# Kernel tuning notes

Hardware: AMD Instinct MI355X
Metric: run time of the kernel (lower is better)

The kernel has to match this reference:

```python
import jax, jax.numpy as jnp
import numpy as np

B, P, CD, RD, H, NR, OD, T = 1024, 22, 256, 64, 512, 12, 2, 100
IN = OD + 2 + CD + RD  # 324: [pos(2), ball(2), context(256), role_embed(64)]


def setup_inputs() -> dict:
    key = jax.random.key(0)
    ks = jax.random.split(key, 20)
    def n(k, shape, s=1.0):
        return jax.random.normal(k, shape, dtype=jnp.float32) * s
    sH = 1.0 / np.sqrt(H)
    sI = 1.0 / np.sqrt(IN)
    return {
        "context": n(ks[0], (B, P, CD)),
        "initial_position": n(ks[1], (B, P, OD)),
        "ball_landing": n(ks[2], (B, 2)),
        "roles": jax.random.randint(ks[3], (B, P), 0, NR, dtype=jnp.int32),
        "max_steps": T,
        "role_table": n(ks[4], (NR, RD), 0.02),
        # LSTM layer 0 (input_dim=IN)
        "W_ih0": n(ks[5], (4 * H, IN), sI),
        "W_hh0": n(ks[6], (4 * H, H), sH),
        "b0": n(ks[7], (4 * H,), sH),  # b_ih + b_hh fused
        # LSTM layer 1 (input_dim=H)
        "W_ih1": n(ks[8], (4 * H, H), sH),
        "W_hh1": n(ks[9], (4 * H, H), sH),
        "b1": n(ks[10], (4 * H,), sH),
        # output MLP: H -> H//2 -> OD
        "W_fc1": n(ks[11], (H // 2, H), sH),
        "b_fc1": n(ks[12], (H // 2,), sH),
        "W_fc2": n(ks[13], (OD, H // 2), 1.0 / np.sqrt(H // 2)),
        "b_fc2": n(ks[14], (OD,), 0.02),
        # initial_pos_encoder: Linear(OD, H)
        "W_init": n(ks[15], (H, OD), 1.0 / np.sqrt(OD)),
        "b_init": n(ks[16], (H,), 0.02),
    }


def _lstm_cell(x, h, c, W_ih, W_hh, b):
    # PyTorch gate order: i, f, g, o
    gates = x @ W_ih.T + h @ W_hh.T + b  # [N, 4H]
    i, f, g, o = jnp.split(gates, 4, axis=-1)
    c_new = jax.nn.sigmoid(f) * c + jax.nn.sigmoid(i) * jnp.tanh(g)
    h_new = jax.nn.sigmoid(o) * jnp.tanh(c_new)
    return h_new, c_new


def reference(context, initial_position, ball_landing, roles, max_steps,
              role_table, W_ih0, W_hh0, b0, W_ih1, W_hh1, b1,
              W_fc1, b_fc1, W_fc2, b_fc2, W_init, b_init):
    batch, num_players, context_dim = context.shape
    N = batch * num_players
    out_dim = initial_position.shape[-1]

    ctx_flat = context.reshape(N, context_dim)
    role_flat = role_table[roles].reshape(N, -1)
    ball_flat = jnp.broadcast_to(ball_landing[:, None, :], (batch, num_players, 2)).reshape(N, 2)
    static = jnp.concatenate([ball_flat, ctx_flat, role_flat], axis=1)  # [N, IN-2]

    pos0 = initial_position.reshape(N, out_dim)
    h0 = pos0 @ W_init.T + b_init  # initial_pos_encoder into layer-0 hidden
    c0 = jnp.zeros_like(h0)
    h1 = jnp.zeros_like(h0)
    c1 = jnp.zeros_like(h0)

    def step(carry, _):
        pos, h0, c0, h1, c1 = carry
        x = jnp.concatenate([pos, static], axis=1)  # [N, IN]
        h0, c0 = _lstm_cell(x, h0, c0, W_ih0, W_hh0, b0)
        h1, c1 = _lstm_cell(h0, h1, c1, W_ih1, W_hh1, b1)
        # output MLP (dropout inactive in eval)
        nxt = jax.nn.relu(h1 @ W_fc1.T + b_fc1) @ W_fc2.T + b_fc2  # [N, OD]
        return (nxt, h0, c0, h1, c1), nxt

    _, preds = jax.lax.scan(step, (pos0, h0, c0, h1, c1), None, length=max_steps)
    # preds: [T, N, OD] -> [batch, num_players, T, OD]
    preds = preds.transpose(1, 0, 2).reshape(batch, num_players, max_steps, out_dim)
    return preds
```

## Files before the change

kernel.cpp:

```cpp
#include <hip/hip_runtime.h>
#include <cstdint>


#define DEVI __device__ __forceinline__

typedef __bf16 bf16x8 __attribute__((ext_vector_type(8)));
typedef float  f32x4  __attribute__((ext_vector_type(4)));
typedef float  f32x2  __attribute__((ext_vector_type(2)));
typedef unsigned short u16x4 __attribute__((ext_vector_type(4)));

static constexpr int NROWS = 22528;
static constexpr int T_STEPS = 100;
static constexpr int NBM = 176;

DEVI unsigned short f2bf(float f) {
  unsigned u = __float_as_uint(f);
  u = u + 0x7FFFu + ((u >> 16) & 1u);
  return (unsigned short)(u >> 16);
}
DEVI float bf2f(unsigned short h) { return __uint_as_float(((unsigned)h) << 16); }

DEVI float fast_sigmoid(float x) {
  float e = __builtin_amdgcn_exp2f(-1.442695041f * x);
  return __builtin_amdgcn_rcpf(1.0f + e);
}
DEVI float fast_tanh(float x) {
  float e = __builtin_amdgcn_exp2f(2.885390082f * x);
  return 1.0f - 2.0f * __builtin_amdgcn_rcpf(e + 1.0f);
}

DEVI void async_copy16(const void* g, void* l) {
  __builtin_amdgcn_global_load_lds(
      (const __attribute__((address_space(1))) void*)g,
      (__attribute__((address_space(3))) void*)l, 16, 0, 0);
}

template <int KITERS, int KSWITCH>
DEVI void gemm_core(const unsigned short* __restrict__ A1, int lda1,
                    const unsigned short* __restrict__ A2, int lda2,
                    const unsigned short* __restrict__ B1, int ldb1,
                    const unsigned short* __restrict__ B2, int ldb2,
                    unsigned short* lds, f32x4 acc[4][4], int tid) {
  const int lane = tid & 63, wid = tid >> 6;
  const int wm = wid & 1, wn = wid >> 1;
  const int c16 = lane & 15, q = lane >> 4;
#pragma unroll
  for (int i = 0; i < 4; ++i)
#pragma unroll
    for (int j = 0; j < 4; ++j) acc[i][j] = f32x4{0.f, 0.f, 0.f, 0.f};
#pragma unroll
  for (int kt = 0; kt < KITERS; ++kt) {
    const bool sec = (kt >= KSWITCH);
    const unsigned short* Ab = sec ? A2 : A1;
    const unsigned short* Bb = sec ? B2 : B1;
    const int lda = sec ? lda2 : lda1;
    const int ldb = sec ? ldb2 : ldb1;
    const int kk = (sec ? (kt - KSWITCH) : kt) * 64;
    __syncthreads();
#pragma unroll
    for (int rd = 0; rd < 4; ++rd) {
      int p = rd * 256 + tid;
      int row = p >> 3, u = p & 7, ch = u ^ (row & 7);
      async_copy16(Ab + row * lda + kk + ch * 8, lds + p * 8);
      async_copy16(Bb + row * ldb + kk + ch * 8, lds + 8192 + p * 8);
    }
    __syncthreads();
#pragma unroll
    for (int s = 0; s < 2; ++s) {
      bf16x8 a[4], b[4];
#pragma unroll
      for (int mf = 0; mf < 4; ++mf) {
        int row = wm * 64 + mf * 16 + c16;
        int slot = row * 8 + ((s * 4 + q) ^ (row & 7));
        a[mf] = *(const bf16x8*)(lds + slot * 8);
      }
#pragma unroll
      for (int nf = 0; nf < 4; ++nf) {
        int row = wn * 64 + nf * 16 + c16;
        int slot = row * 8 + ((s * 4 + q) ^ (row & 7));
        b[nf] = *(const bf16x8*)(lds + 8192 + slot * 8);
      }
#pragma unroll
      for (int mf = 0; mf < 4; ++mf)
#pragma unroll
        for (int nf = 0; nf < 4; ++nf)
          acc[mf][nf] = __builtin_amdgcn_mfma_f32_16x16x32_bf16(a[mf], b[nf], acc[mf][nf], 0, 0, 0);
    }
  }
}

DEVI int orig_row(int j) {
  int tile = j >> 7, rem = j & 127;
  int half = rem >> 6, g = (rem >> 4) & 3, cc = rem & 15;
  return g * 512 + (tile * 32 + half * 16 + cc);
}

__global__ void k_prep_w(const float* __restrict__ Whh0, const float* __restrict__ Wih1,
                         const float* __restrict__ Whh1, const float* __restrict__ Wih0,
                         const float* __restrict__ Wfc1, const float* __restrict__ b0,
                         const float* __restrict__ b1,
                         unsigned short* __restrict__ W0p, unsigned short* __restrict__ Wc1p,
                         unsigned short* __restrict__ Wsp, unsigned short* __restrict__ Wfc1b,
                         float* __restrict__ Wposx, float* __restrict__ Wposy,
                         float* __restrict__ b0p4, float* __restrict__ b1p4) {
  int j = blockIdx.x;
  int k = threadIdx.x;
  int o = orig_row(j);
  W0p[j * 512 + k]         = f2bf(Whh0[o * 512 + k]);
  Wc1p[j * 1024 + k]       = f2bf(Wih1[o * 512 + k]);
  Wc1p[j * 1024 + 512 + k] = f2bf(Whh1[o * 512 + k]);
  if (k < 384) Wsp[j * 384 + k] = (k < 322) ? f2bf(Wih0[o * 324 + 2 + k]) : (unsigned short)0;
  if (k == 0) {
    int g = (j >> 4) & 3;
    int cg = (j >> 7) * 32 + ((j >> 6) & 1) * 16 + (j & 15);
    Wposx[cg * 4 + g] = Wih0[o * 324 + 0];
    Wposy[cg * 4 + g] = Wih0[o * 324 + 1];
    b0p4[cg * 4 + g] = b0[o];
    b1p4[cg * 4 + g] = b1[o];
  }
  if (j < 256) Wfc1b[j * 512 + k] = f2bf(Wfc1[j * 512 + k]);
}

__global__ void k_init_xs(const float* __restrict__ ball, const float* __restrict__ ctx,
                          const int* __restrict__ roles, const float* __restrict__ role_table,
                          unsigned short* __restrict__ Xs) {
  int n = blockIdx.x, col = threadIdx.x;
  int b = n / 22;
  float v;
  if (col < 2)        v = ball[b * 2 + col];
  else if (col < 258) v = ctx[(size_t)n * 256 + col - 2];
  else if (col < 322) v = role_table[roles[n] * 64 + col - 258];
  else                v = 0.f;
  Xs[(size_t)n * 384 + col] = f2bf(v);
}

__global__ void k_init_state(const float* __restrict__ pos0, const float* __restrict__ Winit,
                             const float* __restrict__ binit, unsigned short* __restrict__ Hcat,
                             float* __restrict__ c0, float* __restrict__ c1,
                             float* __restrict__ posb) {
  int idx = blockIdx.x * 256 + threadIdx.x;
  if (idx >= NROWS * 512) return;
  int n = idx >> 9, c = idx & 511;
  float px = pos0[n * 2 + 0], py = pos0[n * 2 + 1];
  float h0 = binit[c] + Winit[c * 2 + 0] * px + Winit[c * 2 + 1] * py;
  Hcat[(size_t)n * 1024 + c] = f2bf(h0);
  Hcat[(size_t)n * 1024 + 512 + c] = 0;
  c0[idx] = 0.f;
  c1[idx] = 0.f;
  if (c < 2) posb[n * 2 + c] = pos0[n * 2 + c];
}

__global__ __launch_bounds__(256) void k_static(const unsigned short* __restrict__ Xs,
                                                const unsigned short* __restrict__ Wsp,
                                                const float* __restrict__ b0p4,
                                                unsigned short* __restrict__ SP2) {
  __shared__ __align__(16) unsigned short lds[16384];
  int tid = threadIdx.x, bn = blockIdx.x, bm = blockIdx.y;
  f32x4 acc[4][4];
  const unsigned short* Ab = Xs + (size_t)bm * 128 * 384;
  const unsigned short* Bb = Wsp + (size_t)bn * 128 * 384;
  gemm_core<6, 6>(Ab, 384, Ab, 384, Bb, 384, Bb, 384, lds, acc, tid);
  int lane = tid & 63, wid = tid >> 6, wm = wid & 1, wn = wid >> 1;
  int c16 = lane & 15, q = lane >> 4;
  int cg = bn * 32 + wn * 16 + c16;
  f32x4 bb = *(const f32x4*)&b0p4[cg * 4];
#pragma unroll
  for (int mf = 0; mf < 4; ++mf) {
    int row0 = bm * 128 + wm * 64 + mf * 16 + q * 4;
#pragma unroll
    for (int r = 0; r < 4; ++r) {
      u16x4 v;
      v.x = f2bf(acc[mf][0][r] + bb.x);
      v.y = f2bf(acc[mf][1][r] + bb.y);
      v.z = f2bf(acc[mf][2][r] + bb.z);
      v.w = f2bf(acc[mf][3][r] + bb.w);
      ((u16x4*)SP2)[(size_t)(row0 + r) * 512 + cg] = v;
    }
  }
}


struct GemmSrc {
  const unsigned short *A1, *A2, *B1, *B2;
  int ldA1, ldA2, ldB1, ldB2;
};

template <int KT, int KSW>
DEVI void stage_q(const GemmSrc& g, int t, int s, int isB, unsigned short* dst, int tid) {
  int tt = (t >= KT) ? (t - 2) : t;
  const bool sec = (tt >= KSW);
  const unsigned short* base;
  int ld;
  if (isB) { base = sec ? g.B2 : g.B1; ld = sec ? g.ldB2 : g.ldB1; }
  else     { base = sec ? g.A2 : g.A1; ld = sec ? g.ldA2 : g.ldA1; }
  base += (sec ? (tt - KSW) : tt) * 64 + s * 32;
#pragma unroll
  for (int rd = 0; rd < 2; ++rd) {
    int p = rd * 512 + tid;
    int row = p >> 2, u = p & 3, ch = u ^ ((row >> 1) & 3);
    async_copy16(base + row * ld + ch * 8, dst + p * 8);
  }
}

#define GBAR   asm volatile("s_barrier" ::: "memory")
#define VMCNT4 asm volatile("s_waitcnt vmcnt(4)" ::: "memory")

template <int KT, int KSW>
DEVI void gemm8(const GemmSrc& g, unsigned short* lds, f32x4 acc[8][4], int tid) {
  const int lane = tid & 63, wid = tid >> 6;
  const int wm = wid >> 2, wn = wid & 3;
  const int c16 = lane & 15, q = lane >> 4;
#pragma unroll
  for (int i = 0; i < 8; ++i)
#pragma unroll
    for (int j = 0; j < 4; ++j) acc[i][j] = f32x4{0.f, 0.f, 0.f, 0.f};
  unsigned short* A00 = lds;
  unsigned short* A01 = lds + 8192;
  unsigned short* B00 = lds + 16384;
  unsigned short* B01 = lds + 24576;
  unsigned short* A10 = lds + 32768;
  unsigned short* A11 = lds + 40960;
  unsigned short* B10 = lds + 49152;
  unsigned short* B11 = lds + 57344;
  const int rowA0 = wm * 128 + c16;
  const int rowB0 = wn * 64 + c16;
  stage_q<KT, KSW>(g, 0, 0, 0, A00, tid);
  stage_q<KT, KSW>(g, 0, 0, 1, B00, tid);
  stage_q<KT, KSW>(g, 0, 1, 0, A01, tid);
  stage_q<KT, KSW>(g, 0, 1, 1, B01, tid);
  stage_q<KT, KSW>(g, 1, 0, 0, A10, tid);
  stage_q<KT, KSW>(g, 1, 0, 1, B10, tid);
  VMCNT4;
  GBAR;
  bf16x8 a[4], b[4];

#define LOADA(BASE, MG)                                                        \
  _Pragma("unroll")                                                            \
  for (int f = 0; f < 4; ++f) {                                                \
    int row = rowA0 + ((MG) * 4 + f) * 16;                                     \
    a[f] = *(const bf16x8*)((BASE) + (row * 4 + (q ^ ((row >> 1) & 3))) * 8);  \
  }
#define LOADB(BASE)                                                            \
  _Pragma("unroll")                                                            \
  for (int f = 0; f < 4; ++f) {                                                \
    int row = rowB0 + f * 16;                                                  \
    b[f] = *(const bf16x8*)((BASE) + (row * 4 + (q ^ ((row >> 1) & 3))) * 8);  \
  }
#define MFG(MG)                                                                \
  __builtin_amdgcn_s_setprio(1);                                               \
  _Pragma("unroll")                                                            \
  for (int f = 0; f < 4; ++f)                                                  \
    _Pragma("unroll")                                                          \
    for (int nf = 0; nf < 4; ++nf)                                             \
      acc[(MG) * 4 + f][nf] = __builtin_amdgcn_mfma_f32_16x16x32_bf16(         \
          a[f], b[nf], acc[(MG) * 4 + f][nf], 0, 0, 0);                        \
  __builtin_amdgcn_s_setprio(0);                                               \
  __builtin_amdgcn_sched_barrier(0);

#pragma unroll 1
  for (int it = 0; it < KT / 2; ++it) {
    const int t0 = 2 * it;
    LOADA(A00, 0); LOADB(B00);
    stage_q<KT, KSW>(g, t0 + 1, 1, 0, A11, tid);
    GBAR; MFG(0); GBAR;
    LOADA(A00, 1);
    stage_q<KT, KSW>(g, t0 + 1, 1, 1, B11, tid);
    GBAR; MFG(1); GBAR;
    LOADA(A01, 0); LOADB(B01);
    stage_q<KT, KSW>(g, t0 + 2, 0, 0, A00, tid);
    GBAR; MFG(0); GBAR;
    LOADA(A01, 1);
    stage_q<KT, KSW>(g, t0 + 2, 0, 1, B00, tid);
    GBAR; MFG(1); VMCNT4; GBAR;
    LOADA(A10, 0); LOADB(B10);
    stage_q<KT, KSW>(g, t0 + 2, 1, 0, A01, tid);
    GBAR; MFG(0); GBAR;
    LOADA(A10, 1);
    stage_q<KT, KSW>(g, t0 + 2, 1, 1, B01, tid);
    GBAR; MFG(1); GBAR;
    LOADA(A11, 0); LOADB(B11);
    stage_q<KT, KSW>(g, t0 + 3, 0, 0, A10, tid);
    GBAR; MFG(0); GBAR;
    LOADA(A11, 1);
    stage_q<KT, KSW>(g, t0 + 3, 0, 1, B10, tid);
    GBAR; MFG(1); VMCNT4; GBAR;
  }
  asm volatile("s_waitcnt vmcnt(0)" ::: "memory");
#undef LOADA
#undef LOADB
#undef MFG
}

DEVI void swz704(int l, int& bn, int& bm) {
  int xcd = l & 7, ii = l >> 3;
  bn = ii & 7;
  bm = (ii >> 3) * 8 + xcd;
}

template <bool USE_SP>
__global__ __launch_bounds__(512, 2) void k_s1_8(const unsigned short* __restrict__ cur,
                                                 const unsigned short* __restrict__ Xs,
                                                 const unsigned short* __restrict__ W0p,
                                                 const unsigned short* __restrict__ Wsp,
                                                 const unsigned short* __restrict__ SP2,
                                                 const float* __restrict__ b0p4,
                                                 const float* __restrict__ Wposx,
                                                 const float* __restrict__ Wposy,
                                                 const float* __restrict__ posb,
                                                 float* __restrict__ c0,
                                                 unsigned short* __restrict__ nxt) {
  __shared__ __align__(16) unsigned short lds[65536];
  const int tid = threadIdx.x;
  int bn, bm;
  swz704(blockIdx.x, bn, bm);
  f32x4 acc[8][4];
  GemmSrc g;
  g.A1 = cur + (size_t)bm * 256 * 1024; g.ldA1 = 1024;
  g.B1 = W0p + (size_t)bn * 256 * 512;  g.ldB1 = 512;
  if constexpr (USE_SP) {
    g.A2 = g.A1; g.ldA2 = 1024; g.B2 = g.B1; g.ldB2 = 512;
    gemm8<8, 8>(g, lds, acc, tid);
  } else {
    g.A2 = Xs + (size_t)bm * 256 * 384;  g.ldA2 = 384;
    g.B2 = Wsp + (size_t)bn * 256 * 384; g.ldB2 = 384;
    gemm8<14, 8>(g, lds, acc, tid);
  }
  const int lane = tid & 63, wid = tid >> 6;
  const int wm = wid >> 2, wn = wid & 3;
  const int c16 = lane & 15, q = lane >> 4;
  const int cg = bn * 64 + (wn >> 1) * 32 + (wn & 1) * 16 + c16;
  f32x4 wpx = *(const f32x4*)&Wposx[cg * 4];
  f32x4 wpy = *(const f32x4*)&Wposy[cg * 4];
  f32x4 sb = f32x4{0.f, 0.f, 0.f, 0.f};
  if constexpr (!USE_SP) sb = *(const f32x4*)&b0p4[cg * 4];
#pragma unroll
  for (int mf = 0; mf < 8; ++mf) {
    int row0 = bm * 256 + wm * 128 + mf * 16 + q * 4;
    f32x4 cold = *(const f32x4*)&c0[(size_t)cg * NROWS + row0];
    f32x4 cnew;
#pragma unroll
    for (int r = 0; r < 4; ++r) {
      size_t row = row0 + r;
      f32x2 pv = *(const f32x2*)&posb[row * 2];
      float s0 = sb.x, s1 = sb.y, s2 = sb.z, s3 = sb.w;
      if constexpr (USE_SP) {
        u16x4 sp = ((const u16x4*)SP2)[row * 512 + cg];
        s0 = bf2f(sp.x); s1 = bf2f(sp.y); s2 = bf2f(sp.z); s3 = bf2f(sp.w);
      }
      float gi = acc[mf][0][r] + s0 + pv.x * wpx.x + pv.y * wpy.x;
      float gf = acc[mf][1][r] + s1 + pv.x * wpx.y + pv.y * wpy.y;
      float gg = acc[mf][2][r] + s2 + pv.x * wpx.z + pv.y * wpy.z;
      float go = acc[mf][3][r] + s3 + pv.x * wpx.w + pv.y * wpy.w;
      float cn = fast_sigmoid(gf) * cold[r] + fast_sigmoid(gi) * fast_tanh(gg);
      cnew[r] = cn;
      nxt[row * 1024 + cg] = f2bf(fast_sigmoid(go) * fast_tanh(cn));
    }
    *(f32x4*)&c0[(size_t)cg * NROWS + row0] = cnew;
  }
}

__global__ __launch_bounds__(512, 2) void k_s2_8(const unsigned short* __restrict__ nxt_in,
                                                 const unsigned short* __restrict__ cur,
                                                 const unsigned short* __restrict__ Wc1p,
                                                 const float* __restrict__ b1p4,
                                                 float* __restrict__ c1,
                                                 unsigned short* __restrict__ nxt_out) {
  __shared__ __align__(16) unsigned short lds[65536];
  const int tid = threadIdx.x;
  int bn, bm;
  swz704(blockIdx.x, bn, bm);
  f32x4 acc[8][4];
  GemmSrc g;
  g.A1 = nxt_in + (size_t)bm * 256 * 1024;      g.ldA1 = 1024;
  g.A2 = cur + (size_t)bm * 256 * 1024 + 512;   g.ldA2 = 1024;
  g.B1 = Wc1p + (size_t)bn * 256 * 1024;        g.ldB1 = 1024;
  g.B2 = g.B1 + 512;                            g.ldB2 = 1024;
  gemm8<16, 8>(g, lds, acc, tid);
  const int lane = tid & 63, wid = tid >> 6;
  const int wm = wid >> 2, wn = wid & 3;
  const int c16 = lane & 15, q = lane >> 4;
  const int cg = bn * 64 + (wn >> 1) * 32 + (wn & 1) * 16 + c16;
  f32x4 bv = *(const f32x4*)&b1p4[cg * 4];
#pragma unroll
  for (int mf = 0; mf < 8; ++mf) {
    int row0 = bm * 256 + wm * 128 + mf * 16 + q * 4;
    f32x4 cold = *(const f32x4*)&c1[(size_t)cg * NROWS + row0];
    f32x4 cnew;
#pragma unroll
    for (int r = 0; r < 4; ++r) {
      size_t row = row0 + r;
      float gi = acc[mf][0][r] + bv.x;
      float gf = acc[mf][1][r] + bv.y;
      float gg = acc[mf][2][r] + bv.z;
      float go = acc[mf][3][r] + bv.w;
      float cn = fast_sigmoid(gf) * cold[r] + fast_sigmoid(gi) * fast_tanh(gg);
      cnew[r] = cn;
      nxt_out[row * 1024 + 512 + cg] = f2bf(fast_sigmoid(go) * fast_tanh(cn));
    }
    *(f32x4*)&c1[(size_t)cg * NROWS + row0] = cnew;
  }
}

__global__ __launch_bounds__(256) void k_s3(const unsigned short* __restrict__ H,
                                            const unsigned short* __restrict__ Wfc1b,
                                            const float* __restrict__ bfc1,
                                            const float* __restrict__ Wfc2,
                                            const float* __restrict__ bfc2,
                                            float* __restrict__ out, float* __restrict__ posb,
                                            int t) {
  __shared__ __align__(16) unsigned short ldsA[32 * 64];
  __shared__ __align__(16) unsigned short ldsB[256 * 64];
  __shared__ float wfc2s[512];
  __shared__ float red[32 * 8];
  int tid = threadIdx.x;
  int l = blockIdx.x, xcd = l & 7, i = l >> 3;
  int b32 = 4 * (xcd + 8 * (i >> 2)) + (i & 3);
  wfc2s[tid] = Wfc2[tid];
  wfc2s[tid + 256] = Wfc2[tid + 256];
  int lane = tid & 63, wid = tid >> 6;
  int c16 = lane & 15, q = lane >> 4;
  f32x4 acc[2][4];
#pragma unroll
  for (int ii = 0; ii < 2; ++ii)
#pragma unroll
    for (int jj = 0; jj < 4; ++jj) acc[ii][jj] = f32x4{0.f, 0.f, 0.f, 0.f};
  const unsigned short* Ab = H + (size_t)b32 * 32 * 1024 + 512;
#pragma unroll
  for (int kt = 0; kt < 8; ++kt) {
    int k0 = kt * 64;
    __syncthreads();
    {
      int p = tid;
      int row = p >> 3, u = p & 7, ch = u ^ (row & 7);
      async_copy16(Ab + row * 1024 + k0 + ch * 8, ldsA + p * 8);
    }
#pragma unroll
    for (int rd = 0; rd < 8; ++rd) {
      int p = rd * 256 + tid;
      int row = p >> 3, u = p & 7, ch = u ^ (row & 7);
      async_copy16(Wfc1b + row * 512 + k0 + ch * 8, ldsB + p * 8);
    }
    __syncthreads();
#pragma unroll
    for (int s = 0; s < 2; ++s) {
      bf16x8 a[2], b[4];
#pragma unroll
      for (int mf = 0; mf < 2; ++mf) {
        int row = mf * 16 + c16;
        int slot = row * 8 + ((s * 4 + q) ^ (row & 7));
        a[mf] = *(const bf16x8*)(ldsA + slot * 8);
      }
#pragma unroll
      for (int nf = 0; nf < 4; ++nf) {
        int row = wid * 64 + nf * 16 + c16;
        int slot = row * 8 + ((s * 4 + q) ^ (row & 7));
        b[nf] = *(const bf16x8*)(ldsB + slot * 8);
      }
#pragma unroll
      for (int mf = 0; mf < 2; ++mf)
#pragma unroll
        for (int nf = 0; nf < 4; ++nf)
          acc[mf][nf] = __builtin_amdgcn_mfma_f32_16x16x32_bf16(a[mf], b[nf], acc[mf][nf], 0, 0, 0);
    }
  }
  float part[2][2][4];
#pragma unroll
  for (int d = 0; d < 2; ++d)
#pragma unroll
    for (int mf = 0; mf < 2; ++mf)
#pragma unroll
      for (int r = 0; r < 4; ++r) part[d][mf][r] = 0.f;
#pragma unroll
  for (int nf = 0; nf < 4; ++nf) {
    int col = wid * 64 + nf * 16 + c16;
    float w0 = wfc2s[col], w1 = wfc2s[256 + col], bv = bfc1[col];
#pragma unroll
    for (int mf = 0; mf < 2; ++mf)
#pragma unroll
      for (int r = 0; r < 4; ++r) {
        float v = acc[mf][nf][r] + bv;
        v = v > 0.f ? v : 0.f;
        part[0][mf][r] += v * w0;
        part[1][mf][r] += v * w1;
      }
  }
#pragma unroll
  for (int st = 1; st < 16; st <<= 1)
#pragma unroll
    for (int d = 0; d < 2; ++d)
#pragma unroll
      for (int mf = 0; mf < 2; ++mf)
#pragma unroll
        for (int r = 0; r < 4; ++r)
          part[d][mf][r] += __shfl_xor(part[d][mf][r], st, 64);
  if (c16 == 0) {
#pragma unroll
    for (int mf = 0; mf < 2; ++mf)
#pragma unroll
      for (int r = 0; r < 4; ++r) {
        int rl = mf * 16 + q * 4 + r;
        red[rl * 8 + wid * 2 + 0] = part[0][mf][r];
        red[rl * 8 + wid * 2 + 1] = part[1][mf][r];
      }
  }
  __syncthreads();
  if (tid < 64) {
    int rl = tid >> 1, d = tid & 1;
    float s = red[rl * 8 + d] + red[rl * 8 + 2 + d] + red[rl * 8 + 4 + d]
            + red[rl * 8 + 6 + d] + bfc2[d];
    int rg = b32 * 32 + rl;
    out[((size_t)rg * T_STEPS + t) * 2 + d] = s;
    posb[rg * 2 + d] = s;
  }
}

extern "C" void kernel_launch(void* const* d_in, const int* in_sizes, int n_in,
                              void* d_out, int out_size, void* d_ws, size_t ws_size,
                              hipStream_t stream) {
  (void)in_sizes; (void)n_in; (void)out_size;
  const float* ctx   = (const float*)d_in[0];
  const float* pos0  = (const float*)d_in[1];
  const float* ball  = (const float*)d_in[2];
  const int*   roles = (const int*)d_in[3];
  const float* role_table = (const float*)d_in[5];
  const float* Wih0 = (const float*)d_in[6];
  const float* Whh0 = (const float*)d_in[7];
  const float* b0   = (const float*)d_in[8];
  const float* Wih1 = (const float*)d_in[9];
  const float* Whh1 = (const float*)d_in[10];
  const float* b1   = (const float*)d_in[11];
  const float* Wfc1 = (const float*)d_in[12];
  const float* bfc1 = (const float*)d_in[13];
  const float* Wfc2 = (const float*)d_in[14];
  const float* bfc2 = (const float*)d_in[15];
  const float* Winit = (const float*)d_in[16];
  const float* binit = (const float*)d_in[17];
  float* out = (float*)d_out;

  char* w = (char*)d_ws;
  size_t used = 0;
  auto alloc = [&](size_t bytes) {
    char* p = w + used;
    used += (bytes + 255) & ~(size_t)255;
    return p;
  };
  unsigned short* W0p   = (unsigned short*)alloc((size_t)2048 * 512 * 2);
  unsigned short* Wc1p  = (unsigned short*)alloc((size_t)2048 * 1024 * 2);
  unsigned short* Wfc1b = (unsigned short*)alloc((size_t)256 * 512 * 2);
  float* Wposx = (float*)alloc(2048 * 4);
  float* Wposy = (float*)alloc(2048 * 4);
  float* b0p4  = (float*)alloc(2048 * 4);
  float* b1p4  = (float*)alloc(2048 * 4);
  float* posb  = (float*)alloc((size_t)NROWS * 2 * 4);
  unsigned short* Hc0 = (unsigned short*)alloc((size_t)NROWS * 1024 * 2);
  float* c0   = (float*)alloc((size_t)NROWS * 512 * 4);
  float* c1   = (float*)alloc((size_t)NROWS * 512 * 4);
  unsigned short* Hc1 = (unsigned short*)alloc((size_t)NROWS * 1024 * 2);

  const size_t SP_BYTES = (size_t)NROWS * 2048 * 2;
  const bool use_sp = (ws_size >= used + SP_BYTES + (1u << 20));

  unsigned short *Xs, *Wsp, *SP2;
  if (use_sp) {
    SP2 = (unsigned short*)alloc(SP_BYTES);
    Xs  = Hc1;
    Wsp = Hc1 + (size_t)NROWS * 384;
  } else {
    SP2 = Hc1;
    Xs  = (unsigned short*)alloc((size_t)NROWS * 384 * 2);
    Wsp = (unsigned short*)alloc((size_t)2048 * 384 * 2);
  }

  k_prep_w<<<2048, 512, 0, stream>>>(Whh0, Wih1, Whh1, Wih0, Wfc1, b0, b1,
                                     W0p, Wc1p, Wsp, Wfc1b, Wposx, Wposy, b0p4, b1p4);
  k_init_xs<<<NROWS, 384, 0, stream>>>(ball, ctx, roles, role_table, Xs);
  k_init_state<<<(NROWS * 512 + 255) / 256, 256, 0, stream>>>(pos0, Winit, binit, Hc0, c0, c1, posb);

  if (use_sp) {
    dim3 gs(16, NBM);
    k_static<<<gs, 256, 0, stream>>>(Xs, Wsp, b0p4, SP2);
  }

  for (int t = 0; t < T_STEPS; ++t) {
    unsigned short* cur = (t & 1) ? Hc1 : Hc0;
    unsigned short* nxt = (t & 1) ? Hc0 : Hc1;
    if (use_sp)
      k_s1_8<true><<<704, 512, 0, stream>>>(cur, Xs, W0p, Wsp, SP2, b0p4,
                                            Wposx, Wposy, posb, c0, nxt);
    else
      k_s1_8<false><<<704, 512, 0, stream>>>(cur, Xs, W0p, Wsp, SP2, b0p4,
                                             Wposx, Wposy, posb, c0, nxt);
    k_s2_8<<<704, 512, 0, stream>>>(nxt, cur, Wc1p, b1p4, c1, nxt);
    k_s3<<<704, 256, 0, stream>>>(nxt, Wfc1b, bfc1, Wfc2, bfc2, out, posb, t);
  }
}
```

Measured before the change: 21.78 ms.

## Prefetch epilogue cell state and SP tiles into LDS during final GEMM iteration

Peels the last K-iteration of the pipelined GEMM. Its now-free stage slots issue async copies of the epilogue operands (the c0/c1 cell-state tile, or the precomputed SP2 static-gate tile) into swizzled LDS. The epilogue then reads these from LDS instead of issuing scattered global loads after the GEMM, so their latency overlaps the last MFMAs. It adds swizzle indexing complexity, a trailing __syncthreads, and a partial fallback to global loads for SP rows that did not fit in LDS.

```diff
diff --git a/kernel.cpp b/kernel.cpp
--- a/kernel.cpp
+++ b/kernel.cpp
@@ -202,11 +202,27 @@
   }
 }
 
+template <int CH0, int W0, int SH, int SH_X>
+DEVI void stage_epi(const char* base, size_t str, unsigned short* lds, int tid) {
+  constexpr int MSK = (1 << SH) - 1;
+  constexpr int MSK_X = (1 << (10 - SH_X < 5 ? 5 : 5)) - 1;
+  (void)MSK_X;
+#pragma unroll
+  for (int rd = 0; rd < 2; ++rd) {
+    int p = rd * 512 + tid;
+    int pos = CH0 + p;
+    int c = pos ^ ((pos >> SH_X) & ((1 << SH_X) - 1) & 31);
+    const char* src = base + (size_t)(c >> SH) * str + (size_t)(c & MSK) * 16;
+    async_copy16(src, lds + W0 + p * 8);
+  }
+}
+
 #define GBAR   asm volatile("s_barrier" ::: "memory")
 #define VMCNT4 asm volatile("s_waitcnt vmcnt(4)" ::: "memory")
 
-template <int KT, int KSW>
-DEVI void gemm8(const GemmSrc& g, unsigned short* lds, f32x4 acc[8][4], int tid) {
+template <int KT, int KSW, int NEPI, int ESH, int ESHX>
+DEVI void gemm8(const GemmSrc& g, const char* eb, size_t estr,
+                unsigned short* lds, f32x4 acc[8][4], int tid) {
   const int lane = tid & 63, wid = tid >> 6;
   const int wm = wid >> 2, wn = wid & 3;
   const int c16 = lane & 15, q = lane >> 4;
@@ -258,7 +274,7 @@
   __builtin_amdgcn_sched_barrier(0);
 
 #pragma unroll 1
-  for (int it = 0; it < KT / 2; ++it) {
+  for (int it = 0; it < KT / 2 - 1; ++it) {
     const int t0 = 2 * it;
     LOADA(A00, 0); LOADB(B00);
     stage_q<KT, KSW>(g, t0 + 1, 1, 0, A11, tid);
@@ -285,7 +301,41 @@
     stage_q<KT, KSW>(g, t0 + 3, 0, 1, B10, tid);
     GBAR; MFG(1); VMCNT4; GBAR;
   }
+  {
+    const int t0 = KT - 2;
+    LOADA(A00, 0); LOADB(B00);
+    stage_q<KT, KSW>(g, t0 + 1, 1, 0, A11, tid);
+    GBAR; MFG(0); GBAR;
+    LOADA(A00, 1);
+    stage_q<KT, KSW>(g, t0 + 1, 1, 1, B11, tid);
+    GBAR; MFG(1); GBAR;
+    LOADA(A01, 0); LOADB(B01);
+    if constexpr (NEPI > 0) stage_epi<0, 0, ESH, ESHX>(eb, estr, lds, tid);
+    else stage_q<KT, KSW>(g, t0 + 2, 0, 0, A00, tid);
+    GBAR; MFG(0); GBAR;
+    LOADA(A01, 1);
+    if constexpr (NEPI > 1) stage_epi<2048, 16384, ESH, ESHX>(eb, estr, lds, tid);
+    else stage_q<KT, KSW>(g, t0 + 2, 0, 1, B00, tid);
+    GBAR; MFG(1); VMCNT4; GBAR;
+    LOADA(A10, 0); LOADB(B10);
+    if constexpr (NEPI > 2) stage_epi<1024, 8192, ESH, ESHX>(eb, estr, lds, tid);
+    else stage_q<KT, KSW>(g, t0 + 2, 1, 0, A01, tid);
+    GBAR; MFG(0); GBAR;
+    LOADA(A10, 1);
+    if constexpr (NEPI > 3) stage_epi<3072, 24576, ESH, ESHX>(eb, estr, lds, tid);
+    else stage_q<KT, KSW>(g, t0 + 2, 1, 1, B01, tid);
+    GBAR; MFG(1); GBAR;
+    LOADA(A11, 0); LOADB(B11);
+    if constexpr (NEPI > 4) stage_epi<4096, 32768, ESH, ESHX>(eb, estr, lds, tid);
+    else stage_q<KT, KSW>(g, t0 + 3, 0, 0, A10, tid);
+    GBAR; MFG(0); GBAR;
+    LOADA(A11, 1);
+    if constexpr (NEPI > 5) stage_epi<5120, 49152, ESH, ESHX>(eb, estr, lds, tid);
+    else stage_q<KT, KSW>(g, t0 + 3, 0, 1, B10, tid);
+    GBAR; MFG(1); VMCNT4; GBAR;
+  }
   asm volatile("s_waitcnt vmcnt(0)" ::: "memory");
+  __syncthreads();
 #undef LOADA
 #undef LOADB
 #undef MFG
@@ -296,6 +346,8 @@
   bn = ii & 7;
   bm = (ii >> 3) * 8 + xcd;
 }
+
+DEVI int epi_word(int j) { return (j < 5) ? (j << 13) : 49152; }
 
 template <bool USE_SP>
 __global__ __launch_bounds__(512, 2) void k_s1_8(const unsigned short* __restrict__ cur,
@@ -319,16 +371,19 @@
   g.B1 = W0p + (size_t)bn * 256 * 512;  g.ldB1 = 512;
   if constexpr (USE_SP) {
     g.A2 = g.A1; g.ldA2 = 1024; g.B2 = g.B1; g.ldB2 = 512;
-    gemm8<8, 8>(g, lds, acc, tid);
+    const char* eb = (const char*)SP2 + ((size_t)(bm * 256) * 512 + (size_t)bn * 64) * 8;
+    gemm8<8, 8, 6, 5, 5>(g, eb, 4096, lds, acc, tid);
   } else {
     g.A2 = Xs + (size_t)bm * 256 * 384;  g.ldA2 = 384;
     g.B2 = Wsp + (size_t)bn * 256 * 384; g.ldB2 = 384;
-    gemm8<14, 8>(g, lds, acc, tid);
+    const char* eb = (const char*)c0 + ((size_t)bn * 64 * NROWS + (size_t)bm * 256) * 4;
+    gemm8<14, 8, 4, 6, 6>(g, eb, (size_t)NROWS * 4, lds, acc, tid);
   }
   const int lane = tid & 63, wid = tid >> 6;
   const int wm = wid >> 2, wn = wid & 3;
   const int c16 = lane & 15, q = lane >> 4;
-  const int cg = bn * 64 + (wn >> 1) * 32 + (wn & 1) * 16 + c16;
+  const int cgl = (wn >> 1) * 32 + (wn & 1) * 16 + c16;
+  const int cg = bn * 64 + cgl;
   f32x4 wpx = *(const f32x4*)&Wposx[cg * 4];
   f32x4 wpy = *(const f32x4*)&Wposy[cg * 4];
   f32x4 sb = f32x4{0.f, 0.f, 0.f, 0.f};
@@ -336,7 +391,14 @@
 #pragma unroll
   for (int mf = 0; mf < 8; ++mf) {
     int row0 = bm * 256 + wm * 128 + mf * 16 + q * 4;
-    f32x4 cold = *(const f32x4*)&c0[(size_t)cg * NROWS + row0];
+    f32x4 cold;
+    if constexpr (USE_SP) {
+      cold = *(const f32x4*)&c0[(size_t)cg * NROWS + row0];
+    } else {
+      int cc = cgl * 64 + wm * 32 + mf * 4 + q;
+      int pos = cc ^ ((cc >> 6) & 63 & 31);
+      cold = *(const f32x4*)(lds + epi_word(pos >> 10) + (pos & 1023) * 8);
+    }
     f32x4 cnew;
 #pragma unroll
     for (int r = 0; r < 4; ++r) {
@@ -344,7 +406,15 @@
       f32x2 pv = *(const f32x2*)&posb[row * 2];
       float s0 = sb.x, s1 = sb.y, s2 = sb.z, s3 = sb.w;
       if constexpr (USE_SP) {
-        u16x4 sp = ((const u16x4*)SP2)[row * 512 + cg];
+        u16x4 sp;
+        if (!(wm == 1 && mf >= 4)) {
+          int lrow = wm * 128 + mf * 16 + q * 4 + r;
+          int cc = lrow * 32 + (cgl >> 1);
+          int pos = cc ^ ((cc >> 5) & 31);
+          sp = *(const u16x4*)(lds + epi_word(pos >> 10) + (pos & 1023) * 8 + ((cgl & 1) << 2));
+        } else {
+          sp = ((const u16x4*)SP2)[row * 512 + cg];
+        }
         s0 = bf2f(sp.x); s1 = bf2f(sp.y); s2 = bf2f(sp.z); s3 = bf2f(sp.w);
       }
       float gi = acc[mf][0][r] + s0 + pv.x * wpx.x + pv.y * wpy.x;
@@ -375,16 +445,20 @@
   g.A2 = cur + (size_t)bm * 256 * 1024 + 512;   g.ldA2 = 1024;
   g.B1 = Wc1p + (size_t)bn * 256 * 1024;        g.ldB1 = 1024;
   g.B2 = g.B1 + 512;                            g.ldB2 = 1024;
-  gemm8<16, 8>(g, lds, acc, tid);
+  const char* eb = (const char*)c1 + ((size_t)bn * 64 * NROWS + (size_t)bm * 256) * 4;
+  gemm8<16, 8, 4, 6, 6>(g, eb, (size_t)NROWS * 4, lds, acc, tid);
   const int lane = tid & 63, wid = tid >> 6;
   const int wm = wid >> 2, wn = wid & 3;
   const int c16 = lane & 15, q = lane >> 4;
-  const int cg = bn * 64 + (wn >> 1) * 32 + (wn & 1) * 16 + c16;
+  const int cgl = (wn >> 1) * 32 + (wn & 1) * 16 + c16;
+  const int cg = bn * 64 + cgl;
   f32x4 bv = *(const f32x4*)&b1p4[cg * 4];
 #pragma unroll
   for (int mf = 0; mf < 8; ++mf) {
     int row0 = bm * 256 + wm * 128 + mf * 16 + q * 4;
-    f32x4 cold = *(const f32x4*)&c1[(size_t)cg * NROWS + row0];
+    int cc = cgl * 64 + wm * 32 + mf * 4 + q;
+    int pos = cc ^ ((cc >> 6) & 63 & 31);
+    f32x4 cold = *(const f32x4*)(lds + epi_word(pos >> 10) + (pos & 1023) * 8);
     f32x4 cnew;
 #pragma unroll
     for (int r = 0; r < 4; ++r) {
```

Measured after the change: 21.87 ms. No clear change (+0.4%).

## Fuse per-step LSTM kernels into one persistent cooperative kernel with grid syncs

Applied to the files above, without the earlier changes.

Replaces the 300 per-timestep kernel launches (layer-0 cell, layer-1 cell, output MLP) with a single cooperative kernel of 256 blocks. It loops over all timesteps and separates the stages with grid-wide syncs and thread fences. Stage bodies become noinline device functions, and blocks stride over the 704 GEMM tiles and 352 MLP tile pairs. This removes launch gaps, but runs one 512-thread block per CU instead of up to two, adds grid-barrier cost, and may hurt register allocation through the noinline calls. It falls back to the old launch loop if the cooperative launch fails.

```diff
diff --git a/kernel.cpp b/kernel.cpp
--- a/kernel.cpp
+++ b/kernel.cpp
@@ -1,5 +1,8 @@
 #include <hip/hip_runtime.h>
+#include <hip/hip_cooperative_groups.h>
 #include <cstdint>
+
+namespace cg = cooperative_groups;
 
 
 #define DEVI __device__ __forceinline__
@@ -178,7 +181,6 @@
     }
   }
 }
-
 
 struct GemmSrc {
   const unsigned short *A1, *A2, *B1, *B2;
@@ -298,21 +300,14 @@
 }
 
 template <bool USE_SP>
-__global__ __launch_bounds__(512, 2) void k_s1_8(const unsigned short* __restrict__ cur,
-                                                 const unsigned short* __restrict__ Xs,
-                                                 const unsigned short* __restrict__ W0p,
-                                                 const unsigned short* __restrict__ Wsp,
-                                                 const unsigned short* __restrict__ SP2,
-                                                 const float* __restrict__ b0p4,
-                                                 const float* __restrict__ Wposx,
-                                                 const float* __restrict__ Wposy,
-                                                 const float* __restrict__ posb,
-                                                 float* __restrict__ c0,
-                                                 unsigned short* __restrict__ nxt) {
-  __shared__ __align__(16) unsigned short lds[65536];
-  const int tid = threadIdx.x;
+__device__ __attribute__((noinline)) void s1_tile(
+    int l, const unsigned short* cur, const unsigned short* Xs,
+    const unsigned short* W0p, const unsigned short* Wsp,
+    const unsigned short* SP2, const float* b0p4,
+    const float* Wposx, const float* Wposy, const float* posb,
+    float* c0, unsigned short* nxt, unsigned short* lds, int tid) {
   int bn, bm;
-  swz704(blockIdx.x, bn, bm);
+  swz704(l, bn, bm);
   f32x4 acc[8][4];
   GemmSrc g;
   g.A1 = cur + (size_t)bm * 256 * 1024; g.ldA1 = 1024;
@@ -359,16 +354,12 @@
   }
 }
 
-__global__ __launch_bounds__(512, 2) void k_s2_8(const unsigned short* __restrict__ nxt_in,
-                                                 const unsigned short* __restrict__ cur,
-                                                 const unsigned short* __restrict__ Wc1p,
-                                                 const float* __restrict__ b1p4,
-                                                 float* __restrict__ c1,
-                                                 unsigned short* __restrict__ nxt_out) {
-  __shared__ __align__(16) unsigned short lds[65536];
-  const int tid = threadIdx.x;
+__device__ __attribute__((noinline)) void s2_tile(
+    int l, const unsigned short* nxt_in, const unsigned short* cur,
+    const unsigned short* Wc1p, const float* b1p4, float* c1,
+    unsigned short* nxt_out, unsigned short* lds, int tid) {
   int bn, bm;
-  swz704(blockIdx.x, bn, bm);
+  swz704(l, bn, bm);
   f32x4 acc[8][4];
   GemmSrc g;
   g.A1 = nxt_in + (size_t)bm * 256 * 1024;      g.ldA1 = 1024;
@@ -401,23 +392,17 @@
   }
 }
 
-__global__ __launch_bounds__(256) void k_s3(const unsigned short* __restrict__ H,
-                                            const unsigned short* __restrict__ Wfc1b,
-                                            const float* __restrict__ bfc1,
-                                            const float* __restrict__ Wfc2,
-                                            const float* __restrict__ bfc2,
-                                            float* __restrict__ out, float* __restrict__ posb,
-                                            int t) {
-  __shared__ __align__(16) unsigned short ldsA[32 * 64];
-  __shared__ __align__(16) unsigned short ldsB[256 * 64];
-  __shared__ float wfc2s[512];
-  __shared__ float red[32 * 8];
-  int tid = threadIdx.x;
-  int l = blockIdx.x, xcd = l & 7, i = l >> 3;
-  int b32 = 4 * (xcd + 8 * (i >> 2)) + (i & 3);
-  wfc2s[tid] = Wfc2[tid];
-  wfc2s[tid + 256] = Wfc2[tid + 256];
-  int lane = tid & 63, wid = tid >> 6;
+__device__ __attribute__((noinline)) void s3_tile(
+    int b32, const unsigned short* H, const unsigned short* Wfc1b,
+    const float* bfc1, const float* Wfc2, const float* bfc2,
+    float* out, float* posb, int t, unsigned short* ldsI, int t256) {
+  unsigned short* ldsA = ldsI;
+  unsigned short* ldsB = ldsI + 2048;
+  float* wfc2s = (float*)(ldsI + 2048 + 16384);
+  float* red   = wfc2s + 512;
+  wfc2s[t256] = Wfc2[t256];
+  wfc2s[t256 + 256] = Wfc2[t256 + 256];
+  int lane = t256 & 63, wid = t256 >> 6;
   int c16 = lane & 15, q = lane >> 4;
   f32x4 acc[2][4];
 #pragma unroll
@@ -430,13 +415,13 @@
     int k0 = kt * 64;
     __syncthreads();
     {
-      int p = tid;
+      int p = t256;
       int row = p >> 3, u = p & 7, ch = u ^ (row & 7);
       async_copy16(Ab + row * 1024 + k0 + ch * 8, ldsA + p * 8);
     }
 #pragma unroll
     for (int rd = 0; rd < 8; ++rd) {
-      int p = rd * 256 + tid;
+      int p = rd * 256 + t256;
       int row = p >> 3, u = p & 7, ch = u ^ (row & 7);
       async_copy16(Wfc1b + row * 512 + k0 + ch * 8, ldsB + p * 8);
     }
@@ -504,14 +489,78 @@
       }
   }
   __syncthreads();
-  if (tid < 64) {
-    int rl = tid >> 1, d = tid & 1;
+  if (t256 < 64) {
+    int rl = t256 >> 1, d = t256 & 1;
     float s = red[rl * 8 + d] + red[rl * 8 + 2 + d] + red[rl * 8 + 4 + d]
             + red[rl * 8 + 6 + d] + bfc2[d];
     int rg = b32 * 32 + rl;
     out[((size_t)rg * T_STEPS + t) * 2 + d] = s;
     posb[rg * 2 + d] = s;
   }
+}
+
+__global__ __launch_bounds__(512, 2) void k_steps(
+    unsigned short* Hc0, unsigned short* Hc1, const unsigned short* Xs,
+    const unsigned short* W0p, const unsigned short* Wsp,
+    const unsigned short* SP2, const float* b0p4,
+    const float* Wposx, const float* Wposy, float* posb, float* c0,
+    const unsigned short* Wc1p, const float* b1p4, float* c1,
+    const unsigned short* Wfc1b, const float* bfc1,
+    const float* Wfc2, const float* bfc2, float* out, int use_sp) {
+  __shared__ __align__(16) unsigned short lds[65536];
+  cg::grid_group grid = cg::this_grid();
+  const int b = blockIdx.x, tid = threadIdx.x;
+  const int inst = tid >> 8, t256 = tid & 255;
+  unsigned short* ldsI = lds + inst * 32768;
+  for (int t = 0; t < T_STEPS; ++t) {
+    unsigned short* cur = (t & 1) ? Hc1 : Hc0;
+    unsigned short* nxt = (t & 1) ? Hc0 : Hc1;
+    for (int l = b; l < 704; l += 256) {
+      if (use_sp) s1_tile<true>(l, cur, Xs, W0p, Wsp, SP2, b0p4, Wposx, Wposy, posb, c0, nxt, lds, tid);
+      else        s1_tile<false>(l, cur, Xs, W0p, Wsp, SP2, b0p4, Wposx, Wposy, posb, c0, nxt, lds, tid);
+    }
+    __threadfence(); grid.sync(); __threadfence();
+    for (int l = b; l < 704; l += 256)
+      s2_tile(l, nxt, cur, Wc1p, b1p4, c1, nxt, lds, tid);
+    __threadfence(); grid.sync(); __threadfence();
+    for (int s = b; s < 352; s += 256)
+      s3_tile(2 * s + inst, nxt, Wfc1b, bfc1, Wfc2, bfc2, out, posb, t, ldsI, t256);
+    __threadfence(); grid.sync(); __threadfence();
+  }
+}
+
+template <bool USE_SP>
+__global__ __launch_bounds__(512, 2) void k_s1_8(const unsigned short* cur,
+                                                 const unsigned short* Xs,
+                                                 const unsigned short* W0p,
+                                                 const unsigned short* Wsp,
+                                                 const unsigned short* SP2,
+                                                 const float* b0p4,
+                                                 const float* Wposx,
+                                                 const float* Wposy,
+                                                 const float* posb,
+                                                 float* c0, unsigned short* nxt) {
+  __shared__ __align__(16) unsigned short lds[65536];
+  s1_tile<USE_SP>(blockIdx.x, cur, Xs, W0p, Wsp, SP2, b0p4, Wposx, Wposy, posb, c0, nxt,
+                  lds, threadIdx.x);
+}
+
+__global__ __launch_bounds__(512, 2) void k_s2_8(const unsigned short* nxt_in,
+                                                 const unsigned short* cur,
+                                                 const unsigned short* Wc1p,
+                                                 const float* b1p4, float* c1,
+                                                 unsigned short* nxt_out) {
+  __shared__ __align__(16) unsigned short lds[65536];
+  s2_tile(blockIdx.x, nxt_in, cur, Wc1p, b1p4, c1, nxt_out, lds, threadIdx.x);
+}
+
+__global__ __launch_bounds__(256) void k_s3(const unsigned short* H,
+                                            const unsigned short* Wfc1b,
+                                            const float* bfc1, const float* Wfc2,
+                                            const float* bfc2, float* out,
+                                            float* posb, int t) {
+  __shared__ __align__(16) unsigned short lds[20480];
+  s3_tile(blockIdx.x, H, Wfc1b, bfc1, Wfc2, bfc2, out, posb, t, lds, threadIdx.x);
 }
 
 extern "C" void kernel_launch(void* const* d_in, const int* in_sizes, int n_in,
@@ -581,16 +630,27 @@
     k_static<<<gs, 256, 0, stream>>>(Xs, Wsp, b0p4, SP2);
   }
 
-  for (int t = 0; t < T_STEPS; ++t) {
-    unsigned short* cur = (t & 1) ? Hc1 : Hc0;
-    unsigned short* nxt = (t & 1) ? Hc0 : Hc1;
-    if (use_sp)
-      k_s1_8<true><<<704, 512, 0, stream>>>(cur, Xs, W0p, Wsp, SP2, b0p4,
-                                            Wposx, Wposy, posb, c0, nxt);
-    else
-      k_s1_8<false><<<704, 512, 0, stream>>>(cur, Xs, W0p, Wsp, SP2, b0p4,
-                                             Wposx, Wposy, posb, c0, nxt);
-    k_s2_8<<<704, 512, 0, stream>>>(nxt, cur, Wc1p, b1p4, c1, nxt);
-    k_s3<<<704, 256, 0, stream>>>(nxt, Wfc1b, bfc1, Wfc2, bfc2, out, posb, t);
-  }
-}
+  int use_sp_i = use_sp ? 1 : 0;
+  void* ka[20] = {
+    (void*)&Hc0, (void*)&Hc1, (void*)&Xs, (void*)&W0p, (void*)&Wsp,
+    (void*)&SP2, (void*)&b0p4, (void*)&Wposx, (void*)&Wposy, (void*)&posb,
+    (void*)&c0, (void*)&Wc1p, (void*)&b1p4, (void*)&c1, (void*)&Wfc1b,
+    (void*)&bfc1, (void*)&Wfc2, (void*)&bfc2, (void*)&out, (void*)&use_sp_i
+  };
+  hipError_t e = hipLaunchCooperativeKernel((const void*)k_steps, dim3(256), dim3(512),
+                                            ka, 0, stream);
+  if (e != hipSuccess) {
+    for (int t = 0; t < T_STEPS; ++t) {
+      unsigned short* cur = (t & 1) ? Hc1 : Hc0;
+      unsigned short* nxt = (t & 1) ? Hc0 : Hc1;
+      if (use_sp)
+        k_s1_8<true><<<704, 512, 0, stream>>>(cur, Xs, W0p, Wsp, SP2, b0p4,
+                                              Wposx, Wposy, posb, c0, nxt);
+      else
+        k_s1_8<false><<<704, 512, 0, stream>>>(cur, Xs, W0p, Wsp, SP2, b0p4,
+                                               Wposx, Wposy, posb, c0, nxt);
+      k_s2_8<<<704, 512, 0, stream>>>(nxt, cur, Wc1p, b1p4, c1, nxt);
+      k_s3<<<704, 256, 0, stream>>>(nxt, Wfc1b, bfc1, Wfc2, bfc2, out, posb, t);
+    }
+  }
+}
```

Measured after the change: 69.93 ms. 221% more time.
